# Performance work log

Measured on AMD Instinct MI355X. Metric: run time of the kernel, lower is better.

The kernel has to match this reference:

```python
import jax, jax.numpy as jnp
import numpy as np

N = 131072      # total nodes (1024 graphs x 128 feature-column nodes)
E = 2097152     # edges (avg degree 16)
G = 1024        # graphs in batch
H = 128         # hidden_dim


def setup_inputs() -> dict:
    key = jax.random.key(0)
    ks = jax.random.split(key, 16)
    s = 0.05
    inp = {
        "x": jax.random.normal(ks[0], (N, 1), dtype=jnp.float32),
        "edge_index": jax.random.randint(ks[1], (2, E), 0, N, dtype=jnp.int64),
        "edge_weight": jax.random.uniform(ks[2], (E,), dtype=jnp.float32),
        "batch": jnp.sort(jax.random.randint(ks[3], (N,), 0, G, dtype=jnp.int64)),
        # GCNConv weights (PyG convention: out = A_hat @ (x @ W) + b)
        "W1": jax.random.normal(ks[4], (1, H), dtype=jnp.float32) * s,
        "b1": jnp.zeros((H,), dtype=jnp.float32),
        "W2": jax.random.normal(ks[5], (H, 2 * H), dtype=jnp.float32) * s,
        "b2": jnp.zeros((2 * H,), dtype=jnp.float32),
        "W3": jax.random.normal(ks[6], (2 * H, H), dtype=jnp.float32) * s,
        "b3": jnp.zeros((H,), dtype=jnp.float32),
        # MLP head
        "Wf1": jax.random.normal(ks[7], (H, 32), dtype=jnp.float32) * s,
        "bf1": jnp.zeros((32,), dtype=jnp.float32),
        "Wf2": jax.random.normal(ks[8], (32, 2), dtype=jnp.float32) * s,
        "bf2": jnp.zeros((2,), dtype=jnp.float32),
    }
    return inp


def reference(x, edge_index, edge_weight, batch, W1, b1, W2, b2, W3, b3, Wf1, bf1, Wf2, bf2):
    # --- GCN normalization with self-loops (gcn_norm, symmetric) ---
    loops = jnp.arange(N, dtype=edge_index.dtype)
    row = jnp.concatenate([edge_index[0], loops])          # src
    col = jnp.concatenate([edge_index[1], loops])          # dst (aggregation target)
    w = jnp.concatenate([edge_weight, jnp.ones((N,), dtype=edge_weight.dtype)])
    deg = jax.ops.segment_sum(w, col, num_segments=N)
    dis = jnp.where(deg > 0, jax.lax.rsqrt(jnp.where(deg > 0, deg, 1.0)), 0.0)
    norm = dis[row] * w * dis[col]                         # [E+N]

    def gcn_conv(h, W, b):
        h = h @ W                                          # [N, out] dense transform
        msg = norm[:, None] * h[row]                       # gather + scale
        return jax.ops.segment_sum(msg, col, num_segments=N) + b

    h = jax.nn.relu(gcn_conv(x, W1, b1))
    h = jax.nn.relu(gcn_conv(h, W2, b2))
    h = jax.nn.relu(gcn_conv(h, W3, b3))

    # --- global_mean_pool over batch segment ids ---
    sums = jax.ops.segment_sum(h, batch, num_segments=G)   # [G, H]
    cnts = jax.ops.segment_sum(jnp.ones((N,), dtype=h.dtype), batch, num_segments=G)
    pooled = sums / jnp.maximum(cnts, 1.0)[:, None]

    # --- MLP head (dropout is identity at inference) ---
    z = jax.nn.relu(pooled @ Wf1 + bf1)
    logits = z @ Wf2 + bf2                                 # [G, 2]
    return logits
```

## Files before the change

kernel.cpp:

```cpp
#include <hip/hip_runtime.h>
#include <math.h>
#include <stdio.h>

#define NN 131072
#define EE 2097152
#define GG 1024
#define NSLICE 256
#define SLICE_SHIFT 9
#define SLICE_N 512
#define NCHUNK 256
#define CHUNK_E (EE / NCHUNK)
#define BCAP 96
#define PSPLIT 4

typedef _Float16 half_t;
typedef _Float16 f16x2 __attribute__((ext_vector_type(2)));
typedef _Float16 f16x4 __attribute__((ext_vector_type(4)));
typedef float f32x4 __attribute__((ext_vector_type(4)));


__global__ __launch_bounds__(256) void k_part(const int* __restrict__ ei,
                                              const float* __restrict__ w,
                                              int* __restrict__ cnts,
                                              uint2* __restrict__ ebuf) {
    __shared__ int cur[NSLICE];
    int t = threadIdx.x, c = blockIdx.x;
    cur[t] = 0;
    __syncthreads();
    int e0 = c * CHUNK_E;
    for (int e = e0 + t; e < e0 + CHUNK_E; e += 256) {
        int d = ei[EE + e];
        int r = ei[e];
        float ww = w[e];
        int b = d >> SLICE_SHIFT;
        int pos = atomicAdd(&cur[b], 1);
        if (pos < BCAP) {
            uint2 p;
            p.x = ((unsigned)(d & (SLICE_N - 1)) << 17) | (unsigned)r;
            p.y = __float_as_uint(ww);
            ebuf[((size_t)c * NSLICE + b) * BCAP + pos] = p;
        }
    }
    __syncthreads();
    cnts[c * NSLICE + t] = min(cur[t], BCAP);
}

__global__ __launch_bounds__(256) void k_stot(const int* __restrict__ cnts,
                                              int* __restrict__ sbase,
                                              int* __restrict__ offs) {
    __shared__ int part[NSLICE];
    int t = threadIdx.x;
    int sum = 0;
    for (int c = 0; c < NCHUNK; ++c) sum += cnts[c * NSLICE + t];
    part[t] = sum;
    __syncthreads();
    for (int off = 1; off < NSLICE; off <<= 1) {
        int v = (t >= off) ? part[t - off] : 0;
        __syncthreads();
        part[t] += v;
        __syncthreads();
    }
    sbase[t] = (t == 0) ? 0 : part[t - 1];
    if (t == NSLICE - 1) offs[NN] = part[NSLICE - 1];
}

__global__ __launch_bounds__(512) void k_slice(const int* __restrict__ cnts,
                                               const uint2* __restrict__ ebuf,
                                               const int* __restrict__ sbase,
                                               const float* __restrict__ x,
                                               int* __restrict__ offs,
                                               float2* __restrict__ xd,
                                               uint2* __restrict__ pairs) {
    __shared__ int hcur[SLICE_N];
    __shared__ float dg[SLICE_N];
    __shared__ int part[512];
    int t = threadIdx.x;
    int s = blockIdx.x;
    int wv = t >> 6, lane = t & 63;
    if (t < SLICE_N) { hcur[t] = 0; dg[t] = 1.0f; }
    __syncthreads();
    for (int c = wv; c < NCHUNK; c += 8) {
        int idx = c * NSLICE + s;
        int cnt = cnts[idx];
        const uint2* base = ebuf + (size_t)idx * BCAP;
        for (int i = lane; i < cnt; i += 64) {
            uint2 e = base[i];
            int dl = e.x >> 17;
            atomicAdd(&hcur[dl], 1);
            atomicAdd(&dg[dl], __uint_as_float(e.y));
        }
    }
    __syncthreads();
    int a = (t < SLICE_N) ? hcur[t] : 0;
    part[t] = a;
    __syncthreads();
    for (int off = 1; off < 512; off <<= 1) {
        int v = (t >= off) ? part[t - off] : 0;
        __syncthreads();
        part[t] += v;
        __syncthreads();
    }
    int ex = (t == 0) ? 0 : part[t - 1];
    int g0 = sbase[s] + ex;
    int nb = s * SLICE_N;
    if (t < SLICE_N) {
        hcur[t] = g0;
        offs[nb + t] = g0;
        float2 v0;
        v0.x = x[nb + t];
        v0.y = rsqrtf(dg[t]);
        xd[nb + t] = v0;
    }
    __syncthreads();
    for (int c = wv; c < NCHUNK; c += 8) {
        int idx = c * NSLICE + s;
        int cnt = cnts[idx];
        const uint2* base = ebuf + (size_t)idx * BCAP;
        for (int i = lane; i < cnt; i += 64) {
            uint2 e = base[i];
            int dl = e.x >> 17;
            int pos = atomicAdd(&hcur[dl], 1);
            uint2 p;
            p.x = e.x & 0x1FFFF;
            p.y = e.y;
            pairs[pos] = p;
        }
    }
}

__global__ __launch_bounds__(256) void k_norm_s(const float2* __restrict__ xd,
                                                const int* __restrict__ offs,
                                                uint2* __restrict__ pairs,
                                                float* __restrict__ sarr) {
    int n = (blockIdx.x * 256 + threadIdx.x) >> 6;
    int lane = threadIdx.x & 63;
    float2 xdn = xd[n];
    float dn = xdn.y;
    int k0 = offs[n], k1 = offs[n + 1];
    float s = 0.f;
    for (int kb = k0; kb < k1; kb += 64) {
        int k = kb + lane;
        if (k < k1) {
            uint2 p = pairs[k];
            float2 xr = xd[p.x];
            float nrm = dn * __uint_as_float(p.y) * xr.y;
            pairs[k].y = __float_as_uint(nrm);
            s = fmaf(nrm, xr.x, s);
        }
    }
#pragma unroll
    for (int off = 32; off > 0; off >>= 1) s += __shfl_xor(s, off);
    if (lane == 0) sarr[n] = fmaf(dn * dn, xdn.x, s);
}

__global__ __launch_bounds__(256) void k_prop0r(const float* __restrict__ sarr,
                                                const float2* __restrict__ xd,
                                                const int* __restrict__ offs,
                                                const uint2* __restrict__ pairs,
                                                const float* __restrict__ W1,
                                                const float* __restrict__ b1,
                                                half_t* __restrict__ Bout) {
    int n = (blockIdx.x * 256 + threadIdx.x) >> 6;
    int lane = threadIdx.x & 63;
    float2 wv = ((const float2*)W1)[lane];
    float2 bv = ((const float2*)b1)[lane];
    float dn = xd[n].y;
    float sn = dn * dn;
    float sown = sarr[n];
    float accx = sn * fmaxf(fmaf(sown, wv.x, bv.x), 0.f);
    float accy = sn * fmaxf(fmaf(sown, wv.y, bv.y), 0.f);
    float ax1 = 0.f, ay1 = 0.f, ax2 = 0.f, ay2 = 0.f, ax3 = 0.f, ay3 = 0.f;
    int k0 = offs[n], k1 = offs[n + 1];
    int k = k0;
    for (; k + 4 <= k1; k += 4) {
        uint2 p0 = pairs[k], p1 = pairs[k + 1], p2 = pairs[k + 2], p3 = pairs[k + 3];
        float s0 = sarr[p0.x], s1 = sarr[p1.x], s2 = sarr[p2.x], s3 = sarr[p3.x];
        float n0 = __uint_as_float(p0.y), n1 = __uint_as_float(p1.y);
        float n2 = __uint_as_float(p2.y), n3 = __uint_as_float(p3.y);
        accx = fmaf(n0, fmaxf(fmaf(s0, wv.x, bv.x), 0.f), accx);
        accy = fmaf(n0, fmaxf(fmaf(s0, wv.y, bv.y), 0.f), accy);
        ax1 = fmaf(n1, fmaxf(fmaf(s1, wv.x, bv.x), 0.f), ax1);
        ay1 = fmaf(n1, fmaxf(fmaf(s1, wv.y, bv.y), 0.f), ay1);
        ax2 = fmaf(n2, fmaxf(fmaf(s2, wv.x, bv.x), 0.f), ax2);
        ay2 = fmaf(n2, fmaxf(fmaf(s2, wv.y, bv.y), 0.f), ay2);
        ax3 = fmaf(n3, fmaxf(fmaf(s3, wv.x, bv.x), 0.f), ax3);
        ay3 = fmaf(n3, fmaxf(fmaf(s3, wv.y, bv.y), 0.f), ay3);
    }
    for (; k < k1; ++k) {
        uint2 p = pairs[k];
        float sv = sarr[p.x];
        float nm = __uint_as_float(p.y);
        accx = fmaf(nm, fmaxf(fmaf(sv, wv.x, bv.x), 0.f), accx);
        accy = fmaf(nm, fmaxf(fmaf(sv, wv.y, bv.y), 0.f), accy);
    }
    accx = (accx + ax1) + (ax2 + ax3);
    accy = (accy + ay1) + (ay2 + ay3);
    f16x2 o;
    o.x = (half_t)accx;
    o.y = (half_t)accy;
    ((f16x2*)Bout)[(size_t)n * 64 + lane] = o;
}

__global__ __launch_bounds__(256) void k_w2p(const float* __restrict__ W2, half_t* __restrict__ W2p) {
    int t = blockIdx.x * 256 + threadIdx.x;
    int slot = t & 3, lane = (t >> 2) & 63, ks = (t >> 8) & 7, nt = t >> 11;
    int col = nt * 16 + (lane & 15);
    int k = ks * 16 + (lane >> 4) * 4 + slot;
    W2p[t] = (half_t)W2[k * 256 + col];
}
__global__ __launch_bounds__(256) void k_w3p(const float* __restrict__ W3, half_t* __restrict__ W3p) {
    int t = blockIdx.x * 256 + threadIdx.x;
    int slot = t & 3, lane = (t >> 2) & 63, ks = (t >> 8) & 15, nt = t >> 12;
    int col = nt * 16 + (lane & 15);
    int k = ks * 16 + (lane >> 4) * 4 + slot;
    W3p[t] = (half_t)W3[k * 128 + col];
}

__global__ __launch_bounds__(256) void k_gemm23(const half_t* __restrict__ Bh,
                                                const half_t* __restrict__ W2p,
                                                const float* __restrict__ b2,
                                                const half_t* __restrict__ W3p,
                                                half_t* __restrict__ Ah) {
    __shared__ __align__(16) char CtB[64 * 512];
    int n0 = blockIdx.x * 64;
    int t = threadIdx.x;
    int wv = t >> 6;
    int lane = t & 63;
    int lr = lane & 15;
    int lc = lane >> 4;

    f16x4 a2[8];
    {
        const char* arow = (const char*)(Bh + (size_t)(n0 + wv * 16 + lr) * 128) + lc * 8;
#pragma unroll
        for (int ks = 0; ks < 8; ++ks)
            a2[ks] = *(const f16x4*)(arow + ks * 32);
    }
    const f16x4* w2f = (const f16x4*)W2p;
    f32x4 acc[16];
#pragma unroll
    for (int nt = 0; nt < 16; ++nt) acc[nt] = (f32x4){0.f, 0.f, 0.f, 0.f};

    f16x4 bcur[16], bnxt[16];
#pragma unroll
    for (int nt = 0; nt < 16; ++nt) bcur[nt] = w2f[(nt * 8 + 0) * 64 + lane];
#pragma unroll
    for (int ks = 0; ks < 8; ++ks) {
        if (ks + 1 < 8) {
#pragma unroll
            for (int nt = 0; nt < 16; ++nt) bnxt[nt] = w2f[(nt * 8 + ks + 1) * 64 + lane];
        }
#pragma unroll
        for (int nt = 0; nt < 16; ++nt)
            acc[nt] = __builtin_amdgcn_mfma_f32_16x16x16f16(a2[ks], bcur[nt], acc[nt], 0, 0, 0);
#pragma unroll
        for (int nt = 0; nt < 16; ++nt) bcur[nt] = bnxt[nt];
    }
#pragma unroll
    for (int nt = 0; nt < 16; ++nt) {
        float bias = b2[nt * 16 + lr];
#pragma unroll
        for (int r = 0; r < 4; ++r) {
            int row = wv * 16 + lc * 4 + r;
            int coff = (nt * 16 + lr) * 2;
            float v = fmaxf(acc[nt][r] + bias, 0.f);
            *(half_t*)(CtB + row * 512 + (coff ^ ((row & 7) << 4))) = (half_t)v;
        }
    }
    __syncthreads();

    f16x4 a3[16];
    {
        int row = wv * 16 + lr;
        const char* rbase = CtB + row * 512;
        int sw = (row & 7) << 4;
#pragma unroll
        for (int ks = 0; ks < 16; ++ks)
            a3[ks] = *(const f16x4*)(rbase + ((ks * 32 + lc * 8) ^ sw));
    }
    const f16x4* w3f = (const f16x4*)W3p;
    f32x4 acc3[8];
#pragma unroll
    for (int nt = 0; nt < 8; ++nt) acc3[nt] = (f32x4){0.f, 0.f, 0.f, 0.f};

    f16x4 ccur[8], cnxt[8];
#pragma unroll
    for (int nt = 0; nt < 8; ++nt) ccur[nt] = w3f[(nt * 16 + 0) * 64 + lane];
#pragma unroll
    for (int ks = 0; ks < 16; ++ks) {
        if (ks + 1 < 16) {
#pragma unroll
            for (int nt = 0; nt < 8; ++nt) cnxt[nt] = w3f[(nt * 16 + ks + 1) * 64 + lane];
        }
#pragma unroll
        for (int nt = 0; nt < 8; ++nt)
            acc3[nt] = __builtin_amdgcn_mfma_f32_16x16x16f16(a3[ks], ccur[nt], acc3[nt], 0, 0, 0);
#pragma unroll
        for (int nt = 0; nt < 8; ++nt) ccur[nt] = cnxt[nt];
    }
#pragma unroll
    for (int nt = 0; nt < 8; ++nt) {
#pragma unroll
        for (int r = 0; r < 4; ++r) {
            int row = n0 + wv * 16 + lc * 4 + r;
            Ah[(size_t)row * 128 + nt * 16 + lr] = (half_t)acc3[nt][r];
        }
    }
}

__global__ __launch_bounds__(256) void k_proppool(const half_t* __restrict__ Ain,
                                                  const float2* __restrict__ xd,
                                                  const int* __restrict__ offs,
                                                  const uint2* __restrict__ pairs,
                                                  const float* __restrict__ b3,
                                                  const int* __restrict__ batch,
                                                  float* __restrict__ ppart) {
    __shared__ float psum[4 * 128];
    int b = blockIdx.x;
    int g = b >> 2, q = b & 3;
    int t = threadIdx.x;
    int wv = t >> 6, lane = t & 63;
    for (int i = t; i < 512; i += 256) psum[i] = 0.f;
    __syncthreads();
    int lo = 0, hi = NN;
    while (lo < hi) { int mid = (lo + hi) >> 1; if (batch[mid] < g) lo = mid + 1; else hi = mid; }
    int s0 = lo;
    lo = s0; hi = NN;
    while (lo < hi) { int mid = (lo + hi) >> 1; if (batch[mid] < g + 1) lo = mid + 1; else hi = mid; }
    int s1 = lo;
    const f16x2* A2 = (const f16x2*)Ain;
    float2 bv = ((const float2*)b3)[lane];
    for (int n = s0 + q * 4 + wv; n < s1; n += 16) {
        float dn = xd[n].y;
        float sn = dn * dn;
        f16x2 av = A2[(size_t)n * 64 + lane];
        float ax0 = sn * (float)av.x, ay0 = sn * (float)av.y;
        float ax1 = 0.f, ay1 = 0.f, ax2 = 0.f, ay2 = 0.f, ax3 = 0.f, ay3 = 0.f;
        int k0 = offs[n], k1 = offs[n + 1];
        int k = k0;
        for (; k + 8 <= k1; k += 8) {
            uint2 p0 = pairs[k],     p1 = pairs[k + 1], p2 = pairs[k + 2], p3 = pairs[k + 3];
            uint2 p4 = pairs[k + 4], p5 = pairs[k + 5], p6 = pairs[k + 6], p7 = pairs[k + 7];
            f16x2 r0 = A2[(size_t)p0.x * 64 + lane];
            f16x2 r1 = A2[(size_t)p1.x * 64 + lane];
            f16x2 r2 = A2[(size_t)p2.x * 64 + lane];
            f16x2 r3 = A2[(size_t)p3.x * 64 + lane];
            f16x2 r4 = A2[(size_t)p4.x * 64 + lane];
            f16x2 r5 = A2[(size_t)p5.x * 64 + lane];
            f16x2 r6 = A2[(size_t)p6.x * 64 + lane];
            f16x2 r7 = A2[(size_t)p7.x * 64 + lane];
            ax0 = fmaf(__uint_as_float(p0.y), (float)r0.x, ax0);
            ay0 = fmaf(__uint_as_float(p0.y), (float)r0.y, ay0);
            ax1 = fmaf(__uint_as_float(p1.y), (float)r1.x, ax1);
            ay1 = fmaf(__uint_as_float(p1.y), (float)r1.y, ay1);
            ax2 = fmaf(__uint_as_float(p2.y), (float)r2.x, ax2);
            ay2 = fmaf(__uint_as_float(p2.y), (float)r2.y, ay2);
            ax3 = fmaf(__uint_as_float(p3.y), (float)r3.x, ax3);
            ay3 = fmaf(__uint_as_float(p3.y), (float)r3.y, ay3);
            ax0 = fmaf(__uint_as_float(p4.y), (float)r4.x, ax0);
            ay0 = fmaf(__uint_as_float(p4.y), (float)r4.y, ay0);
            ax1 = fmaf(__uint_as_float(p5.y), (float)r5.x, ax1);
            ay1 = fmaf(__uint_as_float(p5.y), (float)r5.y, ay1);
            ax2 = fmaf(__uint_as_float(p6.y), (float)r6.x, ax2);
            ay2 = fmaf(__uint_as_float(p6.y), (float)r6.y, ay2);
            ax3 = fmaf(__uint_as_float(p7.y), (float)r7.x, ax3);
            ay3 = fmaf(__uint_as_float(p7.y), (float)r7.y, ay3);
        }
        for (; k + 4 <= k1; k += 4) {
            uint2 p0 = pairs[k], p1 = pairs[k + 1], p2 = pairs[k + 2], p3 = pairs[k + 3];
            f16x2 r0 = A2[(size_t)p0.x * 64 + lane];
            f16x2 r1 = A2[(size_t)p1.x * 64 + lane];
            f16x2 r2 = A2[(size_t)p2.x * 64 + lane];
            f16x2 r3 = A2[(size_t)p3.x * 64 + lane];
            ax0 = fmaf(__uint_as_float(p0.y), (float)r0.x, ax0);
            ay0 = fmaf(__uint_as_float(p0.y), (float)r0.y, ay0);
            ax1 = fmaf(__uint_as_float(p1.y), (float)r1.x, ax1);
            ay1 = fmaf(__uint_as_float(p1.y), (float)r1.y, ay1);
            ax2 = fmaf(__uint_as_float(p2.y), (float)r2.x, ax2);
            ay2 = fmaf(__uint_as_float(p2.y), (float)r2.y, ay2);
            ax3 = fmaf(__uint_as_float(p3.y), (float)r3.x, ax3);
            ay3 = fmaf(__uint_as_float(p3.y), (float)r3.y, ay3);
        }
        for (; k < k1; ++k) {
            uint2 p = pairs[k];
            f16x2 rv = A2[(size_t)p.x * 64 + lane];
            ax0 = fmaf(__uint_as_float(p.y), (float)rv.x, ax0);
            ay0 = fmaf(__uint_as_float(p.y), (float)rv.y, ay0);
        }
        float accx = (ax0 + ax1) + (ax2 + ax3);
        float accy = (ay0 + ay1) + (ay2 + ay3);
        accx = fmaxf(accx + bv.x, 0.f);
        accy = fmaxf(accy + bv.y, 0.f);
        psum[wv * 128 + 2 * lane]     += accx;
        psum[wv * 128 + 2 * lane + 1] += accy;
    }
    __syncthreads();
    if (t < 128) {
        ppart[(size_t)b * 128 + t] = psum[t] + psum[128 + t] + psum[256 + t] + psum[384 + t];
    }
}

__global__ __launch_bounds__(128) void k_pool2(const float* __restrict__ ppart,
                                               const int* __restrict__ batch,
                                               float* __restrict__ pooled) {
    int g = blockIdx.x;
    int t = threadIdx.x;
    int lo = 0, hi = NN;
    while (lo < hi) { int mid = (lo + hi) >> 1; if (batch[mid] < g) lo = mid + 1; else hi = mid; }
    int s0 = lo;
    lo = s0; hi = NN;
    while (lo < hi) { int mid = (lo + hi) >> 1; if (batch[mid] < g + 1) lo = mid + 1; else hi = mid; }
    int s1 = lo;
    float sum = ppart[(size_t)(g * 4 + 0) * 128 + t] + ppart[(size_t)(g * 4 + 1) * 128 + t]
              + ppart[(size_t)(g * 4 + 2) * 128 + t] + ppart[(size_t)(g * 4 + 3) * 128 + t];
    float c = (float)(s1 - s0);
    if (c < 1.f) c = 1.f;
    pooled[g * 128 + t] = sum / c;
}

__global__ __launch_bounds__(128) void k_mlp(const float* __restrict__ pooled,
                                             const float* __restrict__ Wf1,
                                             const float* __restrict__ bf1,
                                             const float* __restrict__ Wf2,
                                             const float* __restrict__ bf2,
                                             float* __restrict__ out) {
    __shared__ float p[128];
    __shared__ float z[32];
    int g = blockIdx.x;
    int t = threadIdx.x;
    p[t] = pooled[g * 128 + t];
    __syncthreads();
    if (t < 32) {
        float a = bf1[t];
        for (int k = 0; k < 128; ++k) a = fmaf(p[k], Wf1[k * 32 + t], a);
        z[t] = fmaxf(a, 0.f);
    }
    __syncthreads();
    if (t < 2) {
        float a = bf2[t];
        for (int j = 0; j < 32; ++j) a = fmaf(z[j], Wf2[j * 2 + t], a);
        out[g * 2 + t] = a;
    }
}

extern "C" void kernel_launch(void* const* d_in, const int* in_sizes, int n_in,
                              void* d_out, int out_size, void* d_ws, size_t ws_size,
                              hipStream_t stream) {
    const float* x   = (const float*)d_in[0];
    const int*   ei  = (const int*)d_in[1];
    const float* w   = (const float*)d_in[2];
    const int*   bat = (const int*)d_in[3];
    const float* W1  = (const float*)d_in[4];
    const float* b1  = (const float*)d_in[5];
    const float* W2  = (const float*)d_in[6];
    const float* b2  = (const float*)d_in[7];
    const float* W3  = (const float*)d_in[8];
    const float* b3  = (const float*)d_in[9];
    const float* Wf1 = (const float*)d_in[10];
    const float* bf1 = (const float*)d_in[11];
    const float* Wf2 = (const float*)d_in[12];
    const float* bf2 = (const float*)d_in[13];
    float* out = (float*)d_out;

    char* ws = (char*)d_ws;
    size_t o = 0;
    auto alloc = [&](size_t bytes) {
        void* p = ws + o;
        o += (bytes + 255) & ~(size_t)255;
        return p;
    };
    int*    offs   = (int*)alloc((size_t)(NN + 1) * 4);
    int*    sbase  = (int*)alloc((size_t)NSLICE * 4);
    int*    cnts   = (int*)alloc((size_t)NCHUNK * NSLICE * 4);
    uint2*  ebuf   = (uint2*)alloc((size_t)NCHUNK * NSLICE * BCAP * 8);
    float2* xd     = (float2*)alloc((size_t)NN * 8);
    float*  sarr   = (float*)alloc((size_t)NN * 4);
    uint2*  pairs  = (uint2*)alloc((size_t)EE * 8);
    half_t* Ah     = (half_t*)alloc((size_t)NN * 128 * 2);
    half_t* Bh     = (half_t*)alloc((size_t)NN * 128 * 2);
    half_t* W2p    = (half_t*)alloc((size_t)256 * 128 * 2);
    half_t* W3p    = (half_t*)alloc((size_t)128 * 256 * 2);
    float*  ppart  = (float*)alloc((size_t)GG * PSPLIT * 128 * 4);
    float*  pooled = (float*)alloc((size_t)GG * 128 * 4);

    if (o > ws_size) {
        fprintf(stderr, "[kernel_launch] ws_size=%zu < needed=%zu — aborting launch\n",
                ws_size, o);
        return;
    }

    k_part<<<NCHUNK, 256, 0, stream>>>(ei, w, cnts, ebuf);
    k_stot<<<1, 256, 0, stream>>>(cnts, sbase, offs);
    k_slice<<<NSLICE, 512, 0, stream>>>(cnts, ebuf, sbase, x, offs, xd, pairs);
    k_w2p<<<128, 256, 0, stream>>>(W2, W2p);
    k_w3p<<<128, 256, 0, stream>>>(W3, W3p);
    k_norm_s<<<NN / 4, 256, 0, stream>>>(xd, offs, pairs, sarr);
    k_prop0r<<<NN / 4, 256, 0, stream>>>(sarr, xd, offs, pairs, W1, b1, Bh);
    k_gemm23<<<NN / 64, 256, 0, stream>>>(Bh, W2p, b2, W3p, Ah);
    k_proppool<<<GG * PSPLIT, 256, 0, stream>>>(Ah, xd, offs, pairs, b3, bat, ppart);
    k_pool2<<<GG, 128, 0, stream>>>(ppart, bat, pooled);
    k_mlp<<<GG, 128, 0, stream>>>(pooled, Wf1, bf1, Wf2, bf2, out);
}
```

Before: 469.1 us.

## Merge weight-pack and pool kernels, double GEMM rows per block, widen pooling split

```diff
diff --git a/kernel.cpp b/kernel.cpp
--- a/kernel.cpp
+++ b/kernel.cpp
@@ -11,7 +11,7 @@
 #define NCHUNK 256
 #define CHUNK_E (EE / NCHUNK)
 #define BCAP 96
-#define PSPLIT 4
+#define PSPLIT 8
 
 typedef _Float16 half_t;
 typedef _Float16 f16x2 __attribute__((ext_vector_type(2)));
@@ -201,19 +201,23 @@
     ((f16x2*)Bout)[(size_t)n * 64 + lane] = o;
 }
 
-__global__ __launch_bounds__(256) void k_w2p(const float* __restrict__ W2, half_t* __restrict__ W2p) {
+__global__ __launch_bounds__(256) void k_wp(const float* __restrict__ W2,
+                                            const float* __restrict__ W3,
+                                            half_t* __restrict__ W2p,
+                                            half_t* __restrict__ W3p) {
     int t = blockIdx.x * 256 + threadIdx.x;
-    int slot = t & 3, lane = (t >> 2) & 63, ks = (t >> 8) & 7, nt = t >> 11;
-    int col = nt * 16 + (lane & 15);
-    int k = ks * 16 + (lane >> 4) * 4 + slot;
-    W2p[t] = (half_t)W2[k * 256 + col];
-}
-__global__ __launch_bounds__(256) void k_w3p(const float* __restrict__ W3, half_t* __restrict__ W3p) {
-    int t = blockIdx.x * 256 + threadIdx.x;
-    int slot = t & 3, lane = (t >> 2) & 63, ks = (t >> 8) & 15, nt = t >> 12;
-    int col = nt * 16 + (lane & 15);
-    int k = ks * 16 + (lane >> 4) * 4 + slot;
-    W3p[t] = (half_t)W3[k * 128 + col];
+    if (t < 32768) {
+        int slot = t & 3, lane = (t >> 2) & 63, ks = (t >> 8) & 7, nt = t >> 11;
+        int col = nt * 16 + (lane & 15);
+        int k = ks * 16 + (lane >> 4) * 4 + slot;
+        W2p[t] = (half_t)W2[k * 256 + col];
+    } else {
+        int u = t - 32768;
+        int slot = u & 3, lane = (u >> 2) & 63, ks = (u >> 8) & 15, nt = u >> 12;
+        int col = nt * 16 + (lane & 15);
+        int k = ks * 16 + (lane >> 4) * 4 + slot;
+        W3p[u] = (half_t)W3[k * 128 + col];
+    }
 }
 
 __global__ __launch_bounds__(256) void k_gemm23(const half_t* __restrict__ Bh,
@@ -221,89 +225,100 @@
                                                 const float* __restrict__ b2,
                                                 const half_t* __restrict__ W3p,
                                                 half_t* __restrict__ Ah) {
-    __shared__ __align__(16) char CtB[64 * 512];
-    int n0 = blockIdx.x * 64;
+    __shared__ __align__(16) char CtB[128 * 512];
+    int n0 = blockIdx.x * 128;
     int t = threadIdx.x;
     int wv = t >> 6;
     int lane = t & 63;
     int lr = lane & 15;
     int lc = lane >> 4;
 
-    f16x4 a2[8];
+    f16x4 aA[8], aB[8];
     {
-        const char* arow = (const char*)(Bh + (size_t)(n0 + wv * 16 + lr) * 128) + lc * 8;
-#pragma unroll
-        for (int ks = 0; ks < 8; ++ks)
-            a2[ks] = *(const f16x4*)(arow + ks * 32);
+        const char* rowA = (const char*)(Bh + (size_t)(n0 + wv * 32 + lr) * 128) + lc * 8;
+        const char* rowB = rowA + 16 * 128 * 2;
+#pragma unroll
+        for (int ks = 0; ks < 8; ++ks) {
+            aA[ks] = *(const f16x4*)(rowA + ks * 32);
+            aB[ks] = *(const f16x4*)(rowB + ks * 32);
+        }
     }
     const f16x4* w2f = (const f16x4*)W2p;
-    f32x4 acc[16];
-#pragma unroll
-    for (int nt = 0; nt < 16; ++nt) acc[nt] = (f32x4){0.f, 0.f, 0.f, 0.f};
-
-    f16x4 bcur[16], bnxt[16];
-#pragma unroll
-    for (int nt = 0; nt < 16; ++nt) bcur[nt] = w2f[(nt * 8 + 0) * 64 + lane];
+    f32x4 accA[16], accB[16];
+#pragma unroll
+    for (int nt = 0; nt < 16; ++nt) {
+        accA[nt] = (f32x4){0.f, 0.f, 0.f, 0.f};
+        accB[nt] = (f32x4){0.f, 0.f, 0.f, 0.f};
+    }
 #pragma unroll
     for (int ks = 0; ks < 8; ++ks) {
-        if (ks + 1 < 8) {
-#pragma unroll
-            for (int nt = 0; nt < 16; ++nt) bnxt[nt] = w2f[(nt * 8 + ks + 1) * 64 + lane];
-        }
-#pragma unroll
-        for (int nt = 0; nt < 16; ++nt)
-            acc[nt] = __builtin_amdgcn_mfma_f32_16x16x16f16(a2[ks], bcur[nt], acc[nt], 0, 0, 0);
-#pragma unroll
-        for (int nt = 0; nt < 16; ++nt) bcur[nt] = bnxt[nt];
+#pragma unroll
+        for (int h = 0; h < 2; ++h) {
+            f16x4 b[8];
+#pragma unroll
+            for (int j = 0; j < 8; ++j) b[j] = w2f[((h * 8 + j) * 8 + ks) * 64 + lane];
+#pragma unroll
+            for (int j = 0; j < 8; ++j) {
+                accA[h * 8 + j] = __builtin_amdgcn_mfma_f32_16x16x16f16(aA[ks], b[j], accA[h * 8 + j], 0, 0, 0);
+                accB[h * 8 + j] = __builtin_amdgcn_mfma_f32_16x16x16f16(aB[ks], b[j], accB[h * 8 + j], 0, 0, 0);
+            }
+        }
     }
 #pragma unroll
     for (int nt = 0; nt < 16; ++nt) {
         float bias = b2[nt * 16 + lr];
+        int coff = (nt * 16 + lr) * 2;
 #pragma unroll
         for (int r = 0; r < 4; ++r) {
-            int row = wv * 16 + lc * 4 + r;
-            int coff = (nt * 16 + lr) * 2;
-            float v = fmaxf(acc[nt][r] + bias, 0.f);
-            *(half_t*)(CtB + row * 512 + (coff ^ ((row & 7) << 4))) = (half_t)v;
-        }
-    }
-    __syncthreads();
-
-    f16x4 a3[16];
+            int rowA_ = wv * 32 + lc * 4 + r;
+            int rowB_ = rowA_ + 16;
+            float vA = fmaxf(accA[nt][r] + bias, 0.f);
+            float vB = fmaxf(accB[nt][r] + bias, 0.f);
+            *(half_t*)(CtB + rowA_ * 512 + (coff ^ ((rowA_ & 7) << 4))) = (half_t)vA;
+            *(half_t*)(CtB + rowB_ * 512 + (coff ^ ((rowB_ & 7) << 4))) = (half_t)vB;
+        }
+    }
+    __syncthreads();
+
+    f16x4 a3A[16], a3B[16];
     {
-        int row = wv * 16 + lr;
-        const char* rbase = CtB + row * 512;
-        int sw = (row & 7) << 4;
-#pragma unroll
-        for (int ks = 0; ks < 16; ++ks)
-            a3[ks] = *(const f16x4*)(rbase + ((ks * 32 + lc * 8) ^ sw));
+        int rowA_ = wv * 32 + lr;
+        int rowB_ = rowA_ + 16;
+        const char* baseA = CtB + rowA_ * 512;
+        const char* baseB = CtB + rowB_ * 512;
+        int swA = (rowA_ & 7) << 4;
+        int swB = (rowB_ & 7) << 4;
+#pragma unroll
+        for (int ks = 0; ks < 16; ++ks) {
+            a3A[ks] = *(const f16x4*)(baseA + ((ks * 32 + lc * 8) ^ swA));
+            a3B[ks] = *(const f16x4*)(baseB + ((ks * 32 + lc * 8) ^ swB));
+        }
     }
     const f16x4* w3f = (const f16x4*)W3p;
-    f32x4 acc3[8];
-#pragma unroll
-    for (int nt = 0; nt < 8; ++nt) acc3[nt] = (f32x4){0.f, 0.f, 0.f, 0.f};
-
-    f16x4 ccur[8], cnxt[8];
-#pragma unroll
-    for (int nt = 0; nt < 8; ++nt) ccur[nt] = w3f[(nt * 16 + 0) * 64 + lane];
+    f32x4 acc3A[8], acc3B[8];
+#pragma unroll
+    for (int nt = 0; nt < 8; ++nt) {
+        acc3A[nt] = (f32x4){0.f, 0.f, 0.f, 0.f};
+        acc3B[nt] = (f32x4){0.f, 0.f, 0.f, 0.f};
+    }
 #pragma unroll
     for (int ks = 0; ks < 16; ++ks) {
-        if (ks + 1 < 16) {
-#pragma unroll
-            for (int nt = 0; nt < 8; ++nt) cnxt[nt] = w3f[(nt * 16 + ks + 1) * 64 + lane];
-        }
-#pragma unroll
-        for (int nt = 0; nt < 8; ++nt)
-            acc3[nt] = __builtin_amdgcn_mfma_f32_16x16x16f16(a3[ks], ccur[nt], acc3[nt], 0, 0, 0);
-#pragma unroll
-        for (int nt = 0; nt < 8; ++nt) ccur[nt] = cnxt[nt];
+        f16x4 cfr[8];
+#pragma unroll
+        for (int nt = 0; nt < 8; ++nt) cfr[nt] = w3f[(nt * 16 + ks) * 64 + lane];
+#pragma unroll
+        for (int nt = 0; nt < 8; ++nt) {
+            acc3A[nt] = __builtin_amdgcn_mfma_f32_16x16x16f16(a3A[ks], cfr[nt], acc3A[nt], 0, 0, 0);
+            acc3B[nt] = __builtin_amdgcn_mfma_f32_16x16x16f16(a3B[ks], cfr[nt], acc3B[nt], 0, 0, 0);
+        }
     }
 #pragma unroll
     for (int nt = 0; nt < 8; ++nt) {
 #pragma unroll
         for (int r = 0; r < 4; ++r) {
-            int row = n0 + wv * 16 + lc * 4 + r;
-            Ah[(size_t)row * 128 + nt * 16 + lr] = (half_t)acc3[nt][r];
+            int rowA_ = n0 + wv * 32 + lc * 4 + r;
+            Ah[(size_t)rowA_ * 128 + nt * 16 + lr] = (half_t)acc3A[nt][r];
+            Ah[(size_t)(rowA_ + 16) * 128 + nt * 16 + lr] = (half_t)acc3B[nt][r];
         }
     }
 }
@@ -317,7 +332,7 @@
                                                   float* __restrict__ ppart) {
     __shared__ float psum[4 * 128];
     int b = blockIdx.x;
-    int g = b >> 2, q = b & 3;
+    int g = b >> 3, q = b & 7;
     int t = threadIdx.x;
     int wv = t >> 6, lane = t & 63;
     for (int i = t; i < 512; i += 256) psum[i] = 0.f;
@@ -330,7 +345,7 @@
     int s1 = lo;
     const f16x2* A2 = (const f16x2*)Ain;
     float2 bv = ((const float2*)b3)[lane];
-    for (int n = s0 + q * 4 + wv; n < s1; n += 16) {
+    for (int n = s0 + q * 4 + wv; n < s1; n += 32) {
         float dn = xd[n].y;
         float sn = dn * dn;
         f16x2 av = A2[(size_t)n * 64 + lane];
@@ -400,25 +415,8 @@
     }
 }
 
-__global__ __launch_bounds__(128) void k_pool2(const float* __restrict__ ppart,
-                                               const int* __restrict__ batch,
-                                               float* __restrict__ pooled) {
-    int g = blockIdx.x;
-    int t = threadIdx.x;
-    int lo = 0, hi = NN;
-    while (lo < hi) { int mid = (lo + hi) >> 1; if (batch[mid] < g) lo = mid + 1; else hi = mid; }
-    int s0 = lo;
-    lo = s0; hi = NN;
-    while (lo < hi) { int mid = (lo + hi) >> 1; if (batch[mid] < g + 1) lo = mid + 1; else hi = mid; }
-    int s1 = lo;
-    float sum = ppart[(size_t)(g * 4 + 0) * 128 + t] + ppart[(size_t)(g * 4 + 1) * 128 + t]
-              + ppart[(size_t)(g * 4 + 2) * 128 + t] + ppart[(size_t)(g * 4 + 3) * 128 + t];
-    float c = (float)(s1 - s0);
-    if (c < 1.f) c = 1.f;
-    pooled[g * 128 + t] = sum / c;
-}
-
-__global__ __launch_bounds__(128) void k_mlp(const float* __restrict__ pooled,
+__global__ __launch_bounds__(128) void k_mlp(const float* __restrict__ ppart,
+                                             const int* __restrict__ batch,
                                              const float* __restrict__ Wf1,
                                              const float* __restrict__ bf1,
                                              const float* __restrict__ Wf2,
@@ -428,7 +426,18 @@
     __shared__ float z[32];
     int g = blockIdx.x;
     int t = threadIdx.x;
-    p[t] = pooled[g * 128 + t];
+    int lo = 0, hi = NN;
+    while (lo < hi) { int mid = (lo + hi) >> 1; if (batch[mid] < g) lo = mid + 1; else hi = mid; }
+    int s0 = lo;
+    lo = s0; hi = NN;
+    while (lo < hi) { int mid = (lo + hi) >> 1; if (batch[mid] < g + 1) lo = mid + 1; else hi = mid; }
+    int s1 = lo;
+    float sum = 0.f;
+#pragma unroll
+    for (int q = 0; q < PSPLIT; ++q) sum += ppart[(size_t)(g * PSPLIT + q) * 128 + t];
+    float c = (float)(s1 - s0);
+    if (c < 1.f) c = 1.f;
+    p[t] = sum / c;
     __syncthreads();
     if (t < 32) {
         float a = bf1[t];
@@ -481,7 +490,6 @@
     half_t* W2p    = (half_t*)alloc((size_t)256 * 128 * 2);
     half_t* W3p    = (half_t*)alloc((size_t)128 * 256 * 2);
     float*  ppart  = (float*)alloc((size_t)GG * PSPLIT * 128 * 4);
-    float*  pooled = (float*)alloc((size_t)GG * 128 * 4);
 
     if (o > ws_size) {
         fprintf(stderr, "[kernel_launch] ws_size=%zu < needed=%zu — aborting launch\n",
@@ -492,12 +500,10 @@
     k_part<<<NCHUNK, 256, 0, stream>>>(ei, w, cnts, ebuf);
     k_stot<<<1, 256, 0, stream>>>(cnts, sbase, offs);
     k_slice<<<NSLICE, 512, 0, stream>>>(cnts, ebuf, sbase, x, offs, xd, pairs);
-    k_w2p<<<128, 256, 0, stream>>>(W2, W2p);
-    k_w3p<<<128, 256, 0, stream>>>(W3, W3p);
+    k_wp<<<256, 256, 0, stream>>>(W2, W3, W2p, W3p);
     k_norm_s<<<NN / 4, 256, 0, stream>>>(xd, offs, pairs, sarr);
     k_prop0r<<<NN / 4, 256, 0, stream>>>(sarr, xd, offs, pairs, W1, b1, Bh);
-    k_gemm23<<<NN / 64, 256, 0, stream>>>(Bh, W2p, b2, W3p, Ah);
+    k_gemm23<<<NN / 128, 256, 0, stream>>>(Bh, W2p, b2, W3p, Ah);
     k_proppool<<<GG * PSPLIT, 256, 0, stream>>>(Ah, xd, offs, pairs, b3, bat, ppart);
-    k_pool2<<<GG, 128, 0, stream>>>(ppart, bat, pooled);
-    k_mlp<<<GG, 128, 0, stream>>>(pooled, Wf1, bf1, Wf2, bf2, out);
-}
+    k_mlp<<<GG, 128, 0, stream>>>(ppart, bat, Wf1, bf1, Wf2, bf2, out);
+}
```

New measurement: 461.7 us. No clear change (-1.6%).
